# Optimization experiments

Hardware: AMD Instinct MI355X
Metric: run time of the kernel (lower is better)

The kernel has to match this reference:

```python
import jax, jax.numpy as jnp
import numpy as np

B, T, C, HS = 8, 2048, 1024, 64
SCALE = C ** (-0.5)  # NOTE: source scales by C, not head_size
NEG_INF = float('-inf')
NEG_BIG = -1e9


def setup_inputs() -> dict:
    key = jax.random.key(0)
    kV, kK, kQ, kWq, kWk, kWv, kL = jax.random.split(key, 7)
    V = jax.random.normal(kV, (B, T, C), dtype=jnp.float32)
    K = jax.random.normal(kK, (B, T, C), dtype=jnp.float32)
    Q = jax.random.normal(kQ, (B, T, C), dtype=jnp.float32)
    w_scale = 1.0 / np.sqrt(C)
    Wq = jax.random.normal(kWq, (C, HS), dtype=jnp.float32) * w_scale
    Wk = jax.random.normal(kWk, (C, HS), dtype=jnp.float32) * w_scale
    Wv = jax.random.normal(kWv, (C, HS), dtype=jnp.float32) * w_scale
    # padding only at the tail; valid lengths in [T//2, T] so no NaN softmax rows
    lengths = jax.random.randint(kL, (B,), T // 2, T + 1)
    pad_mask = (jnp.arange(T)[None, None, :] >= lengths[:, None, None])  # [B,1,T] bool
    return {"V": V, "K": K, "Q": Q, "Wq": Wq, "Wk": Wk, "Wv": Wv, "pad_mask": pad_mask}


def reference(V, K, Q, Wq, Wk, Wv, pad_mask):
    q = Q @ Wq  # [B,T,HS]
    k = K @ Wk
    v = V @ Wv
    A = jnp.einsum('btd,bsd->bts', q, k) * SCALE  # [B,T,T]
    t = A.shape[1]
    causal = jnp.triu(jnp.ones((t, A.shape[2]), dtype=bool), k=1)  # tril==0
    A = jnp.where(causal[None], NEG_INF, A)
    A = jnp.where(pad_mask, NEG_INF, A)  # mask padded key columns
    A = jnp.where(jnp.swapaxes(pad_mask, -2, -1)[:, :t, :], NEG_BIG, A)  # padded query rows
    A = jax.nn.softmax(A, axis=-1)
    return A @ v  # [B,T,HS]
```

## Files before the change

### kernel.cpp

```cpp
#include <hip/hip_runtime.h>

typedef short bf16x8 __attribute__((ext_vector_type(8)));
typedef float f32x4 __attribute__((ext_vector_type(4)));

#define T_SEQ 2048
#define NB 8
#define NEGB (-1e30f)

__device__ inline unsigned short f2bf(float f) {
  unsigned u = __builtin_bit_cast(unsigned, f);
  u += 0x7FFFu + ((u >> 16) & 1u);
  return (unsigned short)(u >> 16);
}
__device__ inline float bf2f(unsigned short h) {
  unsigned u = ((unsigned)h) << 16;
  return __builtin_bit_cast(float, u);
}
__device__ inline f32x4 mfma16(bf16x8 a, bf16x8 b, f32x4 c) {
  return __builtin_amdgcn_mfma_f32_16x16x32_bf16(a, b, c, 0, 0, 0);
}
__device__ inline bf16x8 pack8(float4 a, float4 b) {
  bf16x8 r;
  r[0] = (short)f2bf(a.x); r[1] = (short)f2bf(a.y);
  r[2] = (short)f2bf(a.z); r[3] = (short)f2bf(a.w);
  r[4] = (short)f2bf(b.x); r[5] = (short)f2bf(b.y);
  r[6] = (short)f2bf(b.z); r[7] = (short)f2bf(b.w);
  return r;
}
__device__ __forceinline__ void gl_lds16(const void* g, void* l) {
  __builtin_amdgcn_global_load_lds(
      (const __attribute__((address_space(1))) void*)g,
      (__attribute__((address_space(3))) void*)l, 16, 0, 0);
}

__global__ void detect_k(const unsigned char* m, int* flag) {
  __shared__ int ones, bad;
  int tid = threadIdx.x;
  if (tid == 0) { ones = 0; bad = 0; }
  __syncthreads();
  int lo = 0, lb = 0;
  for (int i = tid; i < NB * T_SEQ; i += 256) {
    int v = (m[i] != 0);
    lo += v;
    if (i & 3) lb += v;
  }
  atomicAdd(&ones, lo);
  atomicAdd(&bad, lb);
  __syncthreads();
  if (tid == 0) *flag = (ones > 0 && bad == 0) ? 1 : 0;
}

__global__ void lengths_k(const unsigned char* m, const int* flag, int* lengths) {
  int b = blockIdx.x, tid = threadIdx.x;
  int cnt = 0;
  if (*flag) {
    const int* mi = (const int*)m;
    for (int t = tid; t < T_SEQ; t += 256) cnt += (mi[b * T_SEQ + t] == 0);
  } else {
    for (int t = tid; t < T_SEQ; t += 256) cnt += (m[b * T_SEQ + t] == 0);
  }
  for (int off = 32; off >= 1; off >>= 1) cnt += __shfl_xor(cnt, off);
  __shared__ int wsum[4];
  if ((tid & 63) == 0) wsum[tid >> 6] = cnt;
  __syncthreads();
  if (tid == 0) lengths[b] = wsum[0] + wsum[1] + wsum[2] + wsum[3];
}

__global__ void wt_k(const float* Wq, const float* Wk, const float* Wv,
                     unsigned short* wt) {
  int e = blockIdx.x * 256 + threadIdx.x;
  if (e >= 3 * 64 * 1024) return;
  int mi = e >> 16;
  int rem = e & 65535;
  int kk = rem & 1023, n = rem >> 10;
  const float* W = (mi == 0) ? Wq : (mi == 1) ? Wk : Wv;
  wt[e] = f2bf(W[kk * 64 + n]);
}

__global__ __launch_bounds__(512, 6) void proj_k(
    const float* Q, const float* K, const float* V, const unsigned short* wt,
    unsigned short* qo, unsigned short* ko, unsigned short* vTb) {
  __shared__ float xs[2][4096];
  __shared__ unsigned short wss[2][4096];
  int mi = blockIdx.y;
  const float* X = (mi == 0) ? Q : (mi == 1) ? K : V;
  const unsigned short* wtm = wt + mi * 65536;
  int tid = threadIdx.x;
  int w = tid >> 6, lane = tid & 63, l15 = lane & 15, g = lane >> 4;
  int wr = w >> 1, wc = w & 1;
  int r0b = blockIdx.x * 64;

  int segA = w * 2;
  int rowA0 = segA * 4 + (lane >> 4);
  int rowA1 = rowA0 + 4;
  int colA0 = ((lane & 15) ^ (rowA0 & 15)) * 4;
  int colA1 = ((lane & 15) ^ (rowA1 & 15)) * 4;
  const float* srcA0 = X + (size_t)(r0b + rowA0) * 1024 + colA0;
  const float* srcA1 = X + (size_t)(r0b + rowA1) * 1024 + colA1;
  int nW = w * 8 + (lane >> 3);
  int skW = ((lane & 7) ^ (nW & 7)) * 8;
  const unsigned short* srcW = wtm + (size_t)nW * 1024 + skW;

  f32x4 acc[2];
  acc[0] = 0; acc[1] = 0;

#define STAGE(buf, kc2)                                          \
  do {                                                           \
    gl_lds16(srcA0 + (kc2) * 64, &xs[buf][segA * 256]);          \
    gl_lds16(srcA1 + (kc2) * 64, &xs[buf][segA * 256 + 256]);    \
    gl_lds16(srcW + (kc2) * 64, &wss[buf][w * 512]);             \
  } while (0)

  STAGE(0, 0);
  asm volatile("s_waitcnt vmcnt(0)" ::: "memory");
  __syncthreads();

  int arow = wr * 16 + l15;
  const float* xrow_lds;
  for (int kc = 0; kc < 16; ++kc) {
    int cur = kc & 1;
    if (kc < 15) STAGE(cur ^ 1, kc + 1);
    xrow_lds = &xs[cur][arow * 64];
#pragma unroll
    for (int ks = 0; ks < 2; ++ks) {
      int lb0 = ks * 8 + g * 2;
      float4 fa = *(const float4*)&xrow_lds[(lb0 ^ l15) * 4];
      float4 fb = *(const float4*)&xrow_lds[((lb0 + 1) ^ l15) * 4];
      bf16x8 a = pack8(fa, fb);
#pragma unroll
      for (int nt = 0; nt < 2; ++nt) {
        int nrow = wc * 32 + nt * 16 + l15;
        bf16x8 bb = *(const bf16x8*)
            &wss[cur][nrow * 64 + (((ks * 4 + g) ^ (l15 & 7)) * 8)];
        acc[nt] = mfma16(a, bb, acc[nt]);
      }
    }
    if (kc < 15) {
      asm volatile("s_waitcnt vmcnt(0)" ::: "memory");
      __syncthreads();
    }
  }
#undef STAGE

#pragma unroll
  for (int nt = 0; nt < 2; ++nt)
#pragma unroll
    for (int vv = 0; vv < 4; ++vv) {
      int rr = r0b + wr * 16 + g * 4 + vv;
      int c = wc * 32 + nt * 16 + l15;
      float val = acc[nt][vv];
      if (mi == 0) {
        qo[(size_t)rr * 64 + c] = f2bf(val * 0.03125f);
      } else if (mi == 1) {
        ko[(size_t)rr * 64 + c] = f2bf(val);
      } else {
        int bb = rr >> 11, ts = rr & 2047;
        vTb[(((size_t)bb * 64 + (ts >> 5)) * 64 + c) * 32 + (ts & 31)] =
            f2bf(val);
      }
    }
}

__global__ void vmean_k(const unsigned short* vTb, float* vmean) {
  int b = blockIdx.x, tid = threadIdx.x;
  int k8 = tid & 3;
  int d = tid >> 2;
  const unsigned short* base = vTb + (size_t)b * 131072;
  float s = 0.f;
  for (int tt = 0; tt < 64; ++tt) {
    bf16x8 v = *(const bf16x8*)&base[(tt * 64 + d) * 32 + k8 * 8];
#pragma unroll
    for (int i = 0; i < 8; ++i) s += bf2f((unsigned short)v[i]);
  }
  s += __shfl_xor(s, 1);
  s += __shfl_xor(s, 2);
  if (k8 == 0) vmean[b * 64 + d] = s * (1.0f / T_SEQ);
}

__global__ __launch_bounds__(512, 4) void attn_k(
    const unsigned short* q, const unsigned short* k, const unsigned short* vTb,
    const float* vmean, const int* lengths, float* Out) {
  __shared__ unsigned short pL[8][16][40];
  __shared__ unsigned short oP[4][2][16][64];
  __shared__ float mP[4][2][16], lP[4][2][16];

  int id = blockIdx.x;
  int raw = id & 63, b = id >> 6;
  int xx = (raw + 8 * b) & 63;
  int tile = (xx < 32) ? xx : 95 - xx;
  int t0 = tile * 32;

  int tid = threadIdx.x;
  int w = tid >> 6, lane = tid & 63;
  int j = w >> 1, r = w & 1;
  int l15 = lane & 15, g = lane >> 4;
  int t_base = t0 + r * 16;

  const bf16x8* qrow =
      (const bf16x8*)(q + ((size_t)b * T_SEQ + t_base + l15) * 64);
  bf16x8 aq0 = qrow[g];
  bf16x8 aq1 = qrow[4 + g];

  f32x4 o[4];
  float m[4], l[4];
#pragma unroll
  for (int i = 0; i < 4; ++i) { o[i] = 0; m[i] = NEGB; l[i] = 0.f; }

  const bf16x8* kch = (const bf16x8*)k + (size_t)b * T_SEQ * 8;
  const unsigned short* vch = vTb + (size_t)b * 131072;

  int NT = tile + 1;
  int qn = NT >> 2, rem = NT & 3;
  int start = j * qn + (j < rem ? j : rem);
  int end = start + qn + (j < rem ? 1 : 0);
  int capw = ((t_base + 15) >> 5) + 1;
  if (end > capw) end = capw;

  for (int tt = start; tt < end; ++tt) {
    int s0 = tt * 32;
    f32x4 sa0, sa1;
    sa0 = 0; sa1 = 0;
    bf16x8 kb00 = kch[(size_t)(s0 + l15) * 8 + g];
    bf16x8 kb01 = kch[(size_t)(s0 + l15) * 8 + 4 + g];
    bf16x8 kb10 = kch[(size_t)(s0 + 16 + l15) * 8 + g];
    bf16x8 kb11 = kch[(size_t)(s0 + 16 + l15) * 8 + 4 + g];
    sa0 = mfma16(aq0, kb00, sa0);
    sa0 = mfma16(aq1, kb01, sa0);
    sa1 = mfma16(aq0, kb10, sa1);
    sa1 = mfma16(aq1, kb11, sa1);
#pragma unroll
    for (int vv = 0; vv < 4; ++vv) {
      int t = t_base + g * 4 + vv;
      float v0 = (s0 + l15 <= t) ? sa0[vv] : NEGB;
      float v1 = (s0 + 16 + l15 <= t) ? sa1[vv] : NEGB;
      float rm = fmaxf(v0, v1);
#pragma unroll
      for (int off = 8; off >= 1; off >>= 1)
        rm = fmaxf(rm, __shfl_xor(rm, off));
      float mn = fmaxf(m[vv], rm);
      float corr = __expf(m[vv] - mn);
      float p0 = (v0 == NEGB) ? 0.f : __expf(v0 - mn);
      float p1 = (v1 == NEGB) ? 0.f : __expf(v1 - mn);
      float rs = p0 + p1;
#pragma unroll
      for (int off = 8; off >= 1; off >>= 1) rs += __shfl_xor(rs, off);
      l[vv] = l[vv] * corr + rs;
      m[vv] = mn;
#pragma unroll
      for (int nt = 0; nt < 4; ++nt) o[nt][vv] *= corr;
      pL[w][g * 4 + vv][l15] = f2bf(p0);
      pL[w][g * 4 + vv][16 + l15] = f2bf(p1);
    }
    bf16x8 ap = *(const bf16x8*)&pL[w][l15][g * 8];
#pragma unroll
    for (int nt = 0; nt < 4; ++nt) {
      bf16x8 bv =
          *(const bf16x8*)&vch[((size_t)(tt * 64 + nt * 16 + l15)) * 32 + g * 8];
      o[nt] = mfma16(ap, bv, o[nt]);
    }
  }

  __syncthreads();
#pragma unroll
  for (int nt = 0; nt < 4; ++nt)
#pragma unroll
    for (int vv = 0; vv < 4; ++vv)
      oP[j][r][g * 4 + vv][nt * 16 + l15] = f2bf(o[nt][vv]);
  if (l15 == 0) {
#pragma unroll
    for (int vv = 0; vv < 4; ++vv) {
      mP[j][r][g * 4 + vv] = m[vv];
      lP[j][r][g * 4 + vv] = l[vv];
    }
  }
  __syncthreads();

  if (w < 2) {
    int len = lengths[b];
#pragma unroll 4
    for (int row = 0; row < 16; ++row) {
      float m0 = mP[0][w][row], m1 = mP[1][w][row];
      float m2 = mP[2][w][row], m3 = mP[3][w][row];
      float ms = fmaxf(fmaxf(m0, m1), fmaxf(m2, m3));
      float e0 = __expf(m0 - ms), e1 = __expf(m1 - ms);
      float e2 = __expf(m2 - ms), e3 = __expf(m3 - ms);
      float ls = lP[0][w][row] * e0 + lP[1][w][row] * e1 +
                 lP[2][w][row] * e2 + lP[3][w][row] * e3;
      float ov = bf2f(oP[0][w][row][lane]) * e0 +
                 bf2f(oP[1][w][row][lane]) * e1 +
                 bf2f(oP[2][w][row][lane]) * e2 +
                 bf2f(oP[3][w][row][lane]) * e3;
      float val = ov / ls;
      int t = t0 + w * 16 + row;
      if (t >= len) val = vmean[b * 64 + lane];
      Out[((size_t)b * T_SEQ + t) * 64 + lane] = val;
    }
  }
}

extern "C" void kernel_launch(void* const* d_in, const int* in_sizes, int n_in,
                              void* d_out, int out_size, void* d_ws,
                              size_t ws_size, hipStream_t stream) {
  const float* V = (const float*)d_in[0];
  const float* K = (const float*)d_in[1];
  const float* Q = (const float*)d_in[2];
  const float* Wq = (const float*)d_in[3];
  const float* Wk = (const float*)d_in[4];
  const float* Wv = (const float*)d_in[5];
  const unsigned char* mask = (const unsigned char*)d_in[6];
  float* O = (float*)d_out;
  char* ws = (char*)d_ws;

  unsigned short* wt = (unsigned short*)(ws);
  unsigned short* qb = (unsigned short*)(ws + 393216);
  unsigned short* kb = (unsigned short*)(ws + 393216 + 2097152);
  unsigned short* vTb = (unsigned short*)(ws + 393216 + 2 * 2097152);
  float* vmean = (float*)(ws + 393216 + 3 * 2097152);
  int* lengths = (int*)(ws + 393216 + 3 * 2097152 + 2048);
  int* flag = lengths + 8;

  detect_k<<<1, 256, 0, stream>>>(mask, flag);
  lengths_k<<<NB, 256, 0, stream>>>(mask, flag, lengths);
  wt_k<<<768, 256, 0, stream>>>(Wq, Wk, Wv, wt);
  proj_k<<<dim3(256, 3), 512, 0, stream>>>(Q, K, V, wt, qb, kb, vTb);
  vmean_k<<<NB, 256, 0, stream>>>(vTb, vmean);
  attn_k<<<512, 512, 0, stream>>>(qb, kb, vTb, vmean, lengths, O);
}
```

Before: 100.6 us.

## Rewrite projection GEMM as split-K register-direct tiles with LDS reduction

The projection kernel drops its LDS double-buffered global_load_lds staging. Each 256-thread block now computes a 16-row tile, with the four waves splitting K into 256-wide slices and loading X and W fragments directly from global memory into registers under two-stage software prefetching. Partial sums are reduced through shared memory by wave 0, and bf16 packing uses the paired conversion intrinsic. This trades LDS traffic and barriers for more blocks and register pressure, but the W slice is reread once per 16-row tile, which raises global and L2 traffic.

Measured after the change: 135.3 us. 1.34x slower.

```diff
diff --git a/kernel.cpp b/kernel.cpp
--- a/kernel.cpp
+++ b/kernel.cpp
@@ -1,7 +1,10 @@
 #include <hip/hip_runtime.h>
+#include <hip/hip_bf16.h>
 
 typedef short bf16x8 __attribute__((ext_vector_type(8)));
 typedef float f32x4 __attribute__((ext_vector_type(4)));
+typedef unsigned int u32;
+typedef u32 u32x4 __attribute__((ext_vector_type(4)));
 
 #define T_SEQ 2048
 #define NB 8
@@ -16,21 +19,22 @@
   unsigned u = ((unsigned)h) << 16;
   return __builtin_bit_cast(float, u);
 }
+__device__ inline u32 cvt2(float a, float b) {
+  __hip_bfloat162 h = __float22bfloat162_rn(make_float2(a, b));
+  u32 r;
+  __builtin_memcpy(&r, &h, 4);
+  return r;
+}
+__device__ inline bf16x8 packfrag(float4 lo, float4 hi) {
+  u32x4 p;
+  p[0] = cvt2(lo.x, lo.y);
+  p[1] = cvt2(lo.z, lo.w);
+  p[2] = cvt2(hi.x, hi.y);
+  p[3] = cvt2(hi.z, hi.w);
+  return __builtin_bit_cast(bf16x8, p);
+}
 __device__ inline f32x4 mfma16(bf16x8 a, bf16x8 b, f32x4 c) {
   return __builtin_amdgcn_mfma_f32_16x16x32_bf16(a, b, c, 0, 0, 0);
-}
-__device__ inline bf16x8 pack8(float4 a, float4 b) {
-  bf16x8 r;
-  r[0] = (short)f2bf(a.x); r[1] = (short)f2bf(a.y);
-  r[2] = (short)f2bf(a.z); r[3] = (short)f2bf(a.w);
-  r[4] = (short)f2bf(b.x); r[5] = (short)f2bf(b.y);
-  r[6] = (short)f2bf(b.z); r[7] = (short)f2bf(b.w);
-  return r;
-}
-__device__ __forceinline__ void gl_lds16(const void* g, void* l) {
-  __builtin_amdgcn_global_load_lds(
-      (const __attribute__((address_space(1))) void*)g,
-      (__attribute__((address_space(3))) void*)l, 16, 0, 0);
 }
 
 __global__ void detect_k(const unsigned char* m, int* flag) {
@@ -77,88 +81,106 @@
   wt[e] = f2bf(W[kk * 64 + n]);
 }
 
-__global__ __launch_bounds__(512, 6) void proj_k(
+__global__ __launch_bounds__(256, 3) void proj_k(
     const float* Q, const float* K, const float* V, const unsigned short* wt,
     unsigned short* qo, unsigned short* ko, unsigned short* vTb) {
-  __shared__ float xs[2][4096];
-  __shared__ unsigned short wss[2][4096];
+  __shared__ f32x4 red[3][4][64];
   int mi = blockIdx.y;
   const float* X = (mi == 0) ? Q : (mi == 1) ? K : V;
   const unsigned short* wtm = wt + mi * 65536;
   int tid = threadIdx.x;
   int w = tid >> 6, lane = tid & 63, l15 = lane & 15, g = lane >> 4;
-  int wr = w >> 1, wc = w & 1;
-  int r0b = blockIdx.x * 64;
-
-  int segA = w * 2;
-  int rowA0 = segA * 4 + (lane >> 4);
-  int rowA1 = rowA0 + 4;
-  int colA0 = ((lane & 15) ^ (rowA0 & 15)) * 4;
-  int colA1 = ((lane & 15) ^ (rowA1 & 15)) * 4;
-  const float* srcA0 = X + (size_t)(r0b + rowA0) * 1024 + colA0;
-  const float* srcA1 = X + (size_t)(r0b + rowA1) * 1024 + colA1;
-  int nW = w * 8 + (lane >> 3);
-  int skW = ((lane & 7) ^ (nW & 7)) * 8;
-  const unsigned short* srcW = wtm + (size_t)nW * 1024 + skW;
-
-  f32x4 acc[2];
-  acc[0] = 0; acc[1] = 0;
-
-#define STAGE(buf, kc2)                                          \
+  int tile = blockIdx.x;
+  int kw0 = w * 256;
+  const float* xrow = X + (size_t)(tile * 16 + l15) * 1024 + kw0 + g * 8;
+
+  f32x4 acc[4];
+#pragma unroll
+  for (int i = 0; i < 4; ++i) acc[i] = 0;
+
+  float4 xA0, xA1, xA2, xA3, xB0, xB1, xB2, xB3;
+  bf16x8 bA0, bA1, bA2, bA3, bA4, bA5, bA6, bA7;
+  bf16x8 bB0, bB1, bB2, bB3, bB4, bB5, bB6, bB7;
+
+#define LOADX(p0, p1, p2, p3, c)                  \
+  do {                                            \
+    const float* xp = xrow + (c) * 64;            \
+    p0 = *(const float4*)(xp);                    \
+    p1 = *(const float4*)(xp + 4);                \
+    p2 = *(const float4*)(xp + 32);               \
+    p3 = *(const float4*)(xp + 36);               \
+  } while (0)
+#define LOADW(q0, q1, q2, q3, q4, q5, q6, q7, c)                            \
+  do {                                                                      \
+    const unsigned short* wp0 = wtm + (size_t)(l15)*1024 + kw0 + (c)*64 + g * 8; \
+    q0 = *(const bf16x8*)(wp0);                                             \
+    q1 = *(const bf16x8*)(wp0 + 32);                                        \
+    q2 = *(const bf16x8*)(wp0 + 16384);                                     \
+    q3 = *(const bf16x8*)(wp0 + 16384 + 32);                                \
+    q4 = *(const bf16x8*)(wp0 + 32768);                                     \
+    q5 = *(const bf16x8*)(wp0 + 32768 + 32);                                \
+    q6 = *(const bf16x8*)(wp0 + 49152);                                     \
+    q7 = *(const bf16x8*)(wp0 + 49152 + 32);                                \
+  } while (0)
+#define COMPUTE(f0, f1, f2, f3, w0, w1, w2, w3, w4, w5, w6, w7)  \
   do {                                                           \
-    gl_lds16(srcA0 + (kc2) * 64, &xs[buf][segA * 256]);          \
-    gl_lds16(srcA1 + (kc2) * 64, &xs[buf][segA * 256 + 256]);    \
-    gl_lds16(srcW + (kc2) * 64, &wss[buf][w * 512]);             \
+    bf16x8 afr = packfrag(f0, f1);                     \
+    acc[0] = mfma16(afr, w0, acc[0]);                            \
+    acc[1] = mfma16(afr, w2, acc[1]);                            \
+    acc[2] = mfma16(afr, w4, acc[2]);                            \
+    acc[3] = mfma16(afr, w6, acc[3]);                            \
+    afr = packfrag(f2, f3);                            \
+    acc[0] = mfma16(afr, w1, acc[0]);                            \
+    acc[1] = mfma16(afr, w3, acc[1]);                            \
+    acc[2] = mfma16(afr, w5, acc[2]);                            \
+    acc[3] = mfma16(afr, w7, acc[3]);                            \
   } while (0)
 
-  STAGE(0, 0);
-  asm volatile("s_waitcnt vmcnt(0)" ::: "memory");
-  __syncthreads();
-
-  int arow = wr * 16 + l15;
-  const float* xrow_lds;
-  for (int kc = 0; kc < 16; ++kc) {
-    int cur = kc & 1;
-    if (kc < 15) STAGE(cur ^ 1, kc + 1);
-    xrow_lds = &xs[cur][arow * 64];
-#pragma unroll
-    for (int ks = 0; ks < 2; ++ks) {
-      int lb0 = ks * 8 + g * 2;
-      float4 fa = *(const float4*)&xrow_lds[(lb0 ^ l15) * 4];
-      float4 fb = *(const float4*)&xrow_lds[((lb0 + 1) ^ l15) * 4];
-      bf16x8 a = pack8(fa, fb);
-#pragma unroll
-      for (int nt = 0; nt < 2; ++nt) {
-        int nrow = wc * 32 + nt * 16 + l15;
-        bf16x8 bb = *(const bf16x8*)
-            &wss[cur][nrow * 64 + (((ks * 4 + g) ^ (l15 & 7)) * 8)];
-        acc[nt] = mfma16(a, bb, acc[nt]);
+  LOADX(xA0, xA1, xA2, xA3, 0);
+  LOADW(bA0, bA1, bA2, bA3, bA4, bA5, bA6, bA7, 0);
+  LOADX(xB0, xB1, xB2, xB3, 1);
+  LOADW(bB0, bB1, bB2, bB3, bB4, bB5, bB6, bB7, 1);
+  COMPUTE(xA0, xA1, xA2, xA3, bA0, bA1, bA2, bA3, bA4, bA5, bA6, bA7);
+  LOADX(xA0, xA1, xA2, xA3, 2);
+  LOADW(bA0, bA1, bA2, bA3, bA4, bA5, bA6, bA7, 2);
+  COMPUTE(xB0, xB1, xB2, xB3, bB0, bB1, bB2, bB3, bB4, bB5, bB6, bB7);
+  LOADX(xB0, xB1, xB2, xB3, 3);
+  LOADW(bB0, bB1, bB2, bB3, bB4, bB5, bB6, bB7, 3);
+  COMPUTE(xA0, xA1, xA2, xA3, bA0, bA1, bA2, bA3, bA4, bA5, bA6, bA7);
+  COMPUTE(xB0, xB1, xB2, xB3, bB0, bB1, bB2, bB3, bB4, bB5, bB6, bB7);
+#undef COMPUTE
+#undef LOADW
+#undef LOADX
+
+  if (w > 0) {
+#pragma unroll
+    for (int nt = 0; nt < 4; ++nt) red[w - 1][nt][lane] = acc[nt];
+  }
+  __syncthreads();
+  if (w == 0) {
+#pragma unroll
+    for (int nt = 0; nt < 4; ++nt) {
+      f32x4 s = acc[nt];
+      s += red[0][nt][lane];
+      s += red[1][nt][lane];
+      s += red[2][nt][lane];
+#pragma unroll
+      for (int vv = 0; vv < 4; ++vv) {
+        int rr = tile * 16 + g * 4 + vv;
+        int c = nt * 16 + l15;
+        float val = s[vv];
+        if (mi == 0) {
+          qo[(size_t)rr * 64 + c] = f2bf(val * 0.03125f);
+        } else if (mi == 1) {
+          ko[(size_t)rr * 64 + c] = f2bf(val);
+        } else {
+          int bb = rr >> 11, ts = rr & 2047;
+          vTb[(((size_t)bb * 64 + (ts >> 5)) * 64 + c) * 32 + (ts & 31)] =
+              f2bf(val);
+        }
       }
     }
-    if (kc < 15) {
-      asm volatile("s_waitcnt vmcnt(0)" ::: "memory");
-      __syncthreads();
-    }
-  }
-#undef STAGE
-
-#pragma unroll
-  for (int nt = 0; nt < 2; ++nt)
-#pragma unroll
-    for (int vv = 0; vv < 4; ++vv) {
-      int rr = r0b + wr * 16 + g * 4 + vv;
-      int c = wc * 32 + nt * 16 + l15;
-      float val = acc[nt][vv];
-      if (mi == 0) {
-        qo[(size_t)rr * 64 + c] = f2bf(val * 0.03125f);
-      } else if (mi == 1) {
-        ko[(size_t)rr * 64 + c] = f2bf(val);
-      } else {
-        int bb = rr >> 11, ts = rr & 2047;
-        vTb[(((size_t)bb * 64 + (ts >> 5)) * 64 + c) * 32 + (ts & 31)] =
-            f2bf(val);
-      }
-    }
+  }
 }
 
 __global__ void vmean_k(const unsigned short* vTb, float* vmean) {
@@ -322,7 +344,7 @@
   detect_k<<<1, 256, 0, stream>>>(mask, flag);
   lengths_k<<<NB, 256, 0, stream>>>(mask, flag, lengths);
   wt_k<<<768, 256, 0, stream>>>(Wq, Wk, Wv, wt);
-  proj_k<<<dim3(256, 3), 512, 0, stream>>>(Q, K, V, wt, qb, kb, vTb);
+  proj_k<<<dim3(1024, 3), 256, 0, stream>>>(Q, K, V, wt, qb, kb, vTb);
   vmean_k<<<NB, 256, 0, stream>>>(vTb, vmean);
   attn_k<<<512, 512, 0, stream>>>(qb, kb, vTb, vmean, lengths, O);
 }
```

## Overlap projection staging loads with compute and use packed bf16 conversion

Applied to the files above, without the earlier changes.

The projection kernel's double-buffered loop now waits only for the previous stage's loads (vmcnt(3)) before computing, so the next stage's global-to-LDS loads stay in flight during the MFMA work. Raw s_barrier with an explicit lgkmcnt wait replaces the full syncthreads. The float-to-bf16 packing uses the paired hardware conversion instead of manual rounding. The occupancy hint in launch bounds drops from 6 to 4. The vmcnt ordering assumptions carry a correctness risk if the compiler reorders or adds memory ops.

Result: no change. 100.6 us (+0.0%).

```diff
diff --git a/kernel.cpp b/kernel.cpp
--- a/kernel.cpp
+++ b/kernel.cpp
@@ -1,7 +1,10 @@
 #include <hip/hip_runtime.h>
+#include <hip/hip_bf16.h>
 
 typedef short bf16x8 __attribute__((ext_vector_type(8)));
 typedef float f32x4 __attribute__((ext_vector_type(4)));
+typedef unsigned int u32;
+typedef u32 u32x4 __attribute__((ext_vector_type(4)));
 
 #define T_SEQ 2048
 #define NB 8
@@ -16,16 +19,22 @@
   unsigned u = ((unsigned)h) << 16;
   return __builtin_bit_cast(float, u);
 }
+__device__ inline u32 cvt2(float a, float b) {
+  __hip_bfloat162 h = __float22bfloat162_rn(make_float2(a, b));
+  u32 r;
+  __builtin_memcpy(&r, &h, 4);
+  return r;
+}
+__device__ inline bf16x8 pack8(float4 a, float4 b) {
+  u32x4 p;
+  p[0] = cvt2(a.x, a.y);
+  p[1] = cvt2(a.z, a.w);
+  p[2] = cvt2(b.x, b.y);
+  p[3] = cvt2(b.z, b.w);
+  return __builtin_bit_cast(bf16x8, p);
+}
 __device__ inline f32x4 mfma16(bf16x8 a, bf16x8 b, f32x4 c) {
   return __builtin_amdgcn_mfma_f32_16x16x32_bf16(a, b, c, 0, 0, 0);
-}
-__device__ inline bf16x8 pack8(float4 a, float4 b) {
-  bf16x8 r;
-  r[0] = (short)f2bf(a.x); r[1] = (short)f2bf(a.y);
-  r[2] = (short)f2bf(a.z); r[3] = (short)f2bf(a.w);
-  r[4] = (short)f2bf(b.x); r[5] = (short)f2bf(b.y);
-  r[6] = (short)f2bf(b.z); r[7] = (short)f2bf(b.w);
-  return r;
 }
 __device__ __forceinline__ void gl_lds16(const void* g, void* l) {
   __builtin_amdgcn_global_load_lds(
@@ -77,7 +86,7 @@
   wt[e] = f2bf(W[kk * 64 + n]);
 }
 
-__global__ __launch_bounds__(512, 6) void proj_k(
+__global__ __launch_bounds__(512, 4) void proj_k(
     const float* Q, const float* K, const float* V, const unsigned short* wt,
     unsigned short* qo, unsigned short* ko, unsigned short* vTb) {
   __shared__ float xs[2][4096];
@@ -112,20 +121,22 @@
   } while (0)
 
   STAGE(0, 0);
-  asm volatile("s_waitcnt vmcnt(0)" ::: "memory");
-  __syncthreads();
 
   int arow = wr * 16 + l15;
-  const float* xrow_lds;
   for (int kc = 0; kc < 16; ++kc) {
     int cur = kc & 1;
-    if (kc < 15) STAGE(cur ^ 1, kc + 1);
-    xrow_lds = &xs[cur][arow * 64];
+    if (kc < 15) {
+      STAGE(cur ^ 1, kc + 1);
+      asm volatile("s_waitcnt vmcnt(3)" ::: "memory");
+    } else {
+      asm volatile("s_waitcnt vmcnt(0)" ::: "memory");
+    }
+    __builtin_amdgcn_s_barrier();
 #pragma unroll
     for (int ks = 0; ks < 2; ++ks) {
       int lb0 = ks * 8 + g * 2;
-      float4 fa = *(const float4*)&xrow_lds[(lb0 ^ l15) * 4];
-      float4 fb = *(const float4*)&xrow_lds[((lb0 + 1) ^ l15) * 4];
+      float4 fa = *(const float4*)&xs[cur][arow * 64 + ((lb0 ^ l15) * 4)];
+      float4 fb = *(const float4*)&xs[cur][arow * 64 + (((lb0 + 1) ^ l15) * 4)];
       bf16x8 a = pack8(fa, fb);
 #pragma unroll
       for (int nt = 0; nt < 2; ++nt) {
@@ -136,8 +147,8 @@
       }
     }
     if (kc < 15) {
-      asm volatile("s_waitcnt vmcnt(0)" ::: "memory");
-      __syncthreads();
+      asm volatile("s_waitcnt lgkmcnt(0)" ::: "memory");
+      __builtin_amdgcn_s_barrier();
     }
   }
 #undef STAGE
```
